# Kernel optimization log

Hardware: AMD Instinct MI355X
Metric: run time of the kernel (lower is better)

Reference implementation:

```python
import jax, jax.numpy as jnp
import numpy as np

N = 4096
E = 262144
IN_DIM = 256
EDGE_DIM = 16
NUM_ATOM_FEATURES = 16
LATENT_DIM = 128
NUM_BOND_TYPES = 5


def setup_inputs() -> dict:
    key = jax.random.key(0)
    ks = jax.random.split(key, 12)
    inp = {
        's': jax.random.normal(ks[0], (N, IN_DIM), dtype=jnp.float32),
        'e': jax.random.normal(ks[1], (E, EDGE_DIM), dtype=jnp.float32),
        'batch': jnp.zeros((N,), dtype=jnp.int64),
        'edge_index_global': jax.random.randint(ks[2], (2, E), 0, N, dtype=jnp.int64),
        # learned parameters (torch nn.Linear layout: W is [out, in])
        'W_shared': jax.random.normal(ks[3], (IN_DIM, IN_DIM), dtype=jnp.float32) * 0.02,
        'b_shared': jnp.zeros((IN_DIM,), dtype=jnp.float32),
        'W_bond': jax.random.normal(ks[4], (IN_DIM, EDGE_DIM), dtype=jnp.float32) * 0.02,
        'b_bond': jnp.zeros((IN_DIM,), dtype=jnp.float32),
        'W_bonds': jax.random.normal(ks[5], (NUM_BOND_TYPES, IN_DIM), dtype=jnp.float32) * 0.02,
        'b_bonds': jnp.zeros((NUM_BOND_TYPES,), dtype=jnp.float32),
        'W_atoms': jax.random.normal(ks[6], (NUM_ATOM_FEATURES + LATENT_DIM, IN_DIM), dtype=jnp.float32) * 0.02,
        'b_atoms': jnp.zeros((NUM_ATOM_FEATURES + LATENT_DIM,), dtype=jnp.float32),
    }
    return inp


def reference(s, e, batch, edge_index_global,
              W_shared, b_shared, W_bond, b_bond,
              W_bonds, b_bonds, W_atoms, b_atoms):
    # shared_mapping: Linear + SiLU
    s = jax.nn.silu(s @ W_shared.T + b_shared)  # [n, in_dim]
    j = edge_index_global[0]
    i = edge_index_global[1]
    n = s.shape[0]

    # atoms_lin then split into atom-type logits and latent prediction
    atoms_out = s @ W_atoms.T + b_atoms  # [n, num_atom_features + latent_dim]
    atoms_pred = atoms_out[:, :NUM_ATOM_FEATURES]
    latent_pred = atoms_out[:, NUM_ATOM_FEATURES:]

    # dense scatter -> symmetrize -> gather (faithful to the original O(n^2) path)
    e_dense = jnp.zeros((n, n, e.shape[-1]), dtype=e.dtype).at[j, i].set(e)
    e_dense = 0.5 * (e_dense + e_dense.transpose(1, 0, 2))
    e_sym = e_dense[j, i]  # [E, edge_dim]

    # fused gather + bond linear + SiLU + bonds linear
    f = jax.nn.silu(s[i] + s[j] + e_sym @ W_bond.T + b_bond)  # [E, in_dim]
    bonds_pred = f @ W_bonds.T + b_bonds  # [E, num_bond_types]

    return (latent_pred, atoms_pred, bonds_pred)
```

## Files before the change

kernel.cpp:

```cpp
#include <hip/hip_runtime.h>
#include <hip/hip_bf16.h>

#define N_NODES   4096
#define E_EDGES   262144
#define IN_DIM    256
#define EDGE_DIM  16
#define NAF       16
#define LATENT    128
#define NBT       5

#define LATENT_OFF 0
#define ATOMS_OFF  (N_NODES * LATENT)
#define BONDS_OFF  (ATOMS_OFF + N_NODES * NAF)

#define TBITS 20
#define TSIZE (1u << TBITS)
#define TMASK (TSIZE - 1u)

typedef float    f32x4  __attribute__((ext_vector_type(4)));
typedef float    f32x4v __attribute__((ext_vector_type(4)));
typedef short    bf16x8 __attribute__((ext_vector_type(8)));
typedef unsigned u32x2  __attribute__((ext_vector_type(2)));
typedef unsigned u32x4  __attribute__((ext_vector_type(4)));

__device__ __forceinline__ float silu_f(float x) {
    return x / (1.0f + __expf(-x));
}

__device__ __forceinline__ unsigned pack_bf16x2(float lo, float hi) {
#if __has_builtin(__builtin_amdgcn_cvt_pk_bf16_f32)
    typedef __bf16 bf16x2_t __attribute__((ext_vector_type(2)));
    union { bf16x2_t v; unsigned u; } c;
    c.v = __builtin_amdgcn_cvt_pk_bf16_f32(lo, hi);
    return c.u;
#else
    union { float f; unsigned u; } a, b;
    a.f = lo; b.f = hi;
    const unsigned ra = (a.u + 0x7FFFu + ((a.u >> 16) & 1u)) >> 16;
    const unsigned rb = (b.u + 0x7FFFu + ((b.u >> 16) & 1u)) >> 16;
    return ra | (rb << 16);
#endif
}

__device__ __forceinline__ float bf_lo(unsigned u) {
    union { unsigned x; float f; } c; c.x = u << 16; return c.f;
}
__device__ __forceinline__ float bf_hi(unsigned u) {
    union { unsigned x; float f; } c; c.x = u & 0xFFFF0000u; return c.f;
}

__device__ __forceinline__ void gld_lds16(const void* g, void* l) {
    __builtin_amdgcn_global_load_lds(
        (const __attribute__((address_space(1))) unsigned*)g,
        (__attribute__((address_space(3))) unsigned*)l, 16, 0, 0);
}

__device__ __forceinline__ int hlookup(const unsigned long long* __restrict__ tab,
                                       unsigned key) {
    unsigned h = (key * 2654435761u) >> (32 - TBITS);
    while (true) {
        const unsigned long long cur = tab[h];
        if (cur == 0ULL) return -1;
        if ((unsigned)(cur >> 18) == key + 1u) return (int)(cur & 0x3FFFFu);
        h = (h + 1u) & TMASK;
    }
}

__global__ __launch_bounds__(256) void k_prep(const float* __restrict__ s,
                                              const float* __restrict__ Wsh,
                                              const float* __restrict__ bsh,
                                              const float* __restrict__ Wa,
                                              const float* __restrict__ ba,
                                              const int* __restrict__ eidx,
                                              const float* __restrict__ Wb,
                                              const float* __restrict__ bb,
                                              const float* __restrict__ Wbs,
                                              unsigned* __restrict__ sact16,
                                              unsigned long long* __restrict__ tab,
                                              u32x4* __restrict__ A12pre,
                                              float* __restrict__ out) {
    __shared__ float sl[8][32];
    __shared__ float st[8][IN_DIM];
    const int blk = blockIdx.x;
    const int c   = threadIdx.x;

    if (blk >= 512) {
        if (blk < 1536) {
            const int k = (blk - 512) * 256 + c;
            const unsigned j = (unsigned)eidx[k];
            const unsigned i = (unsigned)eidx[E_EDGES + k];
            const unsigned key = (j << 12) | i;
            const unsigned long long mine =
                ((unsigned long long)(key + 1u) << 18) | (unsigned)k;
            unsigned h = (key * 2654435761u) >> (32 - TBITS);
            while (true) {
                unsigned long long cur = tab[h];
                if (cur == 0ULL) {
                    const unsigned long long old = atomicCAS(&tab[h], 0ULL, mine);
                    if (old == 0ULL) return;
                    cur = old;
                }
                if ((unsigned)(cur >> 18) == key + 1u) {
                    atomicMax(&tab[h], mine);
                    return;
                }
                h = (h + 1u) & TMASK;
            }
        } else {
#pragma unroll
            for (int ee = 0; ee < 4; ++ee) {
                const int idx  = c + 256 * ee;
                const int g    = idx >> 6;
                const int lane = idx & 63;
                const int m    = lane & 15;
                const int q    = lane >> 4;

                const float4 w = *(const float4*)(Wb + (16 * g + m) * EDGE_DIM + 4 * q);
                u32x4 r;
                r.x = pack_bf16x2(w.x, w.y);
                r.y = pack_bf16x2(w.z, w.w);
                if (m < NBT) {
                    const float4 ws = *(const float4*)(Wbs + m * IN_DIM + 16 * g + 4 * q);
                    r.z = pack_bf16x2(ws.x, ws.y);
                    r.w = pack_bf16x2(ws.z, ws.w);
                } else {
                    r.z = 0u; r.w = 0u;
                }
                A12pre[idx] = r;
            }
        }
        return;
    }

    const int r0 = blk * 8;

    float acc[8];
    const float bias = bsh[c];
#pragma unroll
    for (int r = 0; r < 8; ++r) acc[r] = bias;

    for (int k0 = 0; k0 < IN_DIM; k0 += 32) {
        sl[c >> 5][c & 31] = s[(r0 + (c >> 5)) * IN_DIM + k0 + (c & 31)];
        __syncthreads();

        float4 w4[8];
        const float4* wp = (const float4*)(Wsh + c * IN_DIM + k0);
#pragma unroll
        for (int q = 0; q < 8; ++q) w4[q] = wp[q];
        const float* wf = (const float*)w4;
#pragma unroll
        for (int r = 0; r < 8; ++r) {
            const float4* srow = (const float4*)sl[r];
            float a = acc[r];
#pragma unroll
            for (int q = 0; q < 8; ++q) {
                const float4 sv = srow[q];
                a += sv.x * wf[q * 4 + 0];
                a += sv.y * wf[q * 4 + 1];
                a += sv.z * wf[q * 4 + 2];
                a += sv.w * wf[q * 4 + 3];
            }
            acc[r] = a;
        }
        __syncthreads();
    }
#pragma unroll
    for (int r = 0; r < 8; ++r) st[r][c] = silu_f(acc[r]);
    __syncthreads();

    if (c < 128) {
        const float b0 = 0.5f * bb[2 * c];
        const float b1 = 0.5f * bb[2 * c + 1];
#pragma unroll
        for (int r = 0; r < 8; ++r)
            sact16[(size_t)(r0 + r) * 128 + c] =
                pack_bf16x2(st[r][2 * c] + b0, st[r][2 * c + 1] + b1);
    }

    const bool active = (c < (NAF + LATENT));
    float acc2[8];
    const float bias2 = active ? ba[c] : 0.0f;
#pragma unroll
    for (int r = 0; r < 8; ++r) acc2[r] = bias2;

    if (active) {
        for (int k0 = 0; k0 < IN_DIM; k0 += 32) {
            float4 w4[8];
            const float4* wp = (const float4*)(Wa + c * IN_DIM + k0);
#pragma unroll
            for (int q = 0; q < 8; ++q) w4[q] = wp[q];
            const float* wf = (const float*)w4;
#pragma unroll
            for (int r = 0; r < 8; ++r) {
                const float4* srow = (const float4*)(st[r] + k0);
                float a = acc2[r];
#pragma unroll
                for (int q = 0; q < 8; ++q) {
                    const float4 sv = srow[q];
                    a += sv.x * wf[q * 4 + 0];
                    a += sv.y * wf[q * 4 + 1];
                    a += sv.z * wf[q * 4 + 2];
                    a += sv.w * wf[q * 4 + 3];
                }
                acc2[r] = a;
            }
        }
#pragma unroll
        for (int r = 0; r < 8; ++r) {
            const int row = r0 + r;
            if (c < NAF) out[ATOMS_OFF + row * NAF + c] = acc2[r];
            else         out[LATENT_OFF + row * LATENT + (c - NAF)] = acc2[r];
        }
    }
}

__global__ __launch_bounds__(256, 5) void k_edges_mfma(const int* __restrict__ eidx,
                                                       const float* __restrict__ e,
                                                       const unsigned long long* __restrict__ tab,
                                                       const unsigned* __restrict__ sact16,
                                                       const u32x4* __restrict__ A12pre,
                                                       const float* __restrict__ bbs,
                                                       float* __restrict__ out) {
    __shared__ unsigned lds_all[4][2048];
    const int lane = threadIdx.x & 63;
    const int wv   = threadIdx.x >> 6;
    const int m    = lane & 15;
    const int q    = lane >> 4;
    const int k0   = __builtin_amdgcn_readfirstlane((blockIdx.x * 4 + wv) * 16);
    unsigned* myl = lds_all[wv];

    f32x4v acc_init;
#pragma unroll
    for (int r = 0; r < 4; ++r) {
        const int bond = 4 * q + r;
        acc_init[r] = (bond < NBT) ? bbs[bond] : 0.0f;
    }

    const unsigned j_m = (unsigned)eidx[k0 + m];
    const unsigned i_m = (unsigned)eidx[E_EDGES + k0 + m];

    const char* si_base = (const char*)(sact16 + (size_t)i_m * 128);
    const char* sj_base = (const char*)(sact16 + (size_t)j_m * 128);

#pragma unroll
    for (int u = 0; u < 4; ++u)
        gld_lds16(si_base + (4 * u + q) * 16, (char*)myl + u * 1024);
#pragma unroll
    for (int u = 0; u < 4; ++u)
        gld_lds16(sj_base + (4 * u + q) * 16, (char*)myl + 4096 + u * 1024);

    const unsigned wf = (unsigned)hlookup(tab, (j_m << 12) | i_m);
    const int      wr = hlookup(tab, (i_m << 12) | j_m);

    f32x4 es = *(const f32x4*)(e + (size_t)wf * EDGE_DIM + 4 * q);
    if (wr >= 0)
        es += *(const f32x4*)(e + (size_t)wr * EDGE_DIM + 4 * q);
    es *= 0.5f;

    union { bf16x8 v; unsigned u[4]; } B1;
    B1.u[0] = pack_bf16x2(es[0], es[1]);
    B1.u[1] = pack_bf16x2(es[2], es[3]);
    B1.u[2] = 0u; B1.u[3] = 0u;

    const u32x4* a12p = A12pre + lane;

    f32x4v acc0 = acc_init;
    f32x4v acc1 = {0.0f, 0.0f, 0.0f, 0.0f};

    const int qh  = q >> 1;
    const int qw  = 2 * (q & 1);
    const int mw  = m * 4;

    auto run_half = [&](int h) {
#pragma unroll
        for (int gp = 0; gp < 8; ++gp) {
            const int g     = 8 * h + gp;
            const int chunk = 2 * gp + qh;
            const int offw  = (chunk >> 2) * 256 + ((chunk & 3) * 16) * 4 + mw + qw;

            const u32x2 wi = *(const u32x2*)(myl + offw);
            const u32x2 wj = *(const u32x2*)(myl + 1024 + offw);

            f32x4v C1;
            C1[0] = bf_lo(wi.x) + bf_lo(wj.x);
            C1[1] = bf_hi(wi.x) + bf_hi(wj.x);
            C1[2] = bf_lo(wi.y) + bf_lo(wj.y);
            C1[3] = bf_hi(wi.y) + bf_hi(wj.y);

            const u32x4 rec = a12p[g * 64];
            union { bf16x8 v; unsigned u[4]; } A1, A2;
            A1.u[0] = rec.x; A1.u[1] = rec.y; A1.u[2] = 0u; A1.u[3] = 0u;
            A2.u[0] = rec.z; A2.u[1] = rec.w; A2.u[2] = 0u; A2.u[3] = 0u;

            const f32x4v P = __builtin_amdgcn_mfma_f32_16x16x32_bf16(A1.v, B1.v, C1, 0, 0, 0);

            union { bf16x8 v; unsigned u[4]; } B2;
            B2.u[0] = pack_bf16x2(silu_f(P[0]), silu_f(P[1]));
            B2.u[1] = pack_bf16x2(silu_f(P[2]), silu_f(P[3]));
            B2.u[2] = 0u; B2.u[3] = 0u;

            if (g & 1) acc1 = __builtin_amdgcn_mfma_f32_16x16x32_bf16(A2.v, B2.v, acc1, 0, 0, 0);
            else       acc0 = __builtin_amdgcn_mfma_f32_16x16x32_bf16(A2.v, B2.v, acc0, 0, 0, 0);
        }
    };

    __asm__ __volatile__("s_waitcnt vmcnt(0)" ::: "memory");
    run_half(0);

    __asm__ __volatile__("s_waitcnt lgkmcnt(0)" ::: "memory");
#pragma unroll
    for (int u = 0; u < 4; ++u)
        gld_lds16(si_base + 256 + (4 * u + q) * 16, (char*)myl + u * 1024);
#pragma unroll
    for (int u = 0; u < 4; ++u)
        gld_lds16(sj_base + 256 + (4 * u + q) * 16, (char*)myl + 4096 + u * 1024);
    __asm__ __volatile__("s_waitcnt vmcnt(0)" ::: "memory");
    run_half(1);

    const f32x4v accT = acc0 + acc1;
    float* op = out + BONDS_OFF + (size_t)(k0 + m) * NBT;
    if (q == 0) {
        __builtin_nontemporal_store(accT[0], op + 0);
        __builtin_nontemporal_store(accT[1], op + 1);
        __builtin_nontemporal_store(accT[2], op + 2);
        __builtin_nontemporal_store(accT[3], op + 3);
    } else if (q == 1) {
        __builtin_nontemporal_store(accT[0], op + 4);
    }
}

extern "C" void kernel_launch(void* const* d_in, const int* in_sizes, int n_in,
                              void* d_out, int out_size, void* d_ws, size_t ws_size,
                              hipStream_t stream) {
    const float* s   = (const float*)d_in[0];
    const float* e   = (const float*)d_in[1];
    const int*   eix = (const int*)d_in[3];
    const float* Wsh = (const float*)d_in[4];
    const float* bsh = (const float*)d_in[5];
    const float* Wb  = (const float*)d_in[6];
    const float* bbo = (const float*)d_in[7];
    const float* Wbs = (const float*)d_in[8];
    const float* bbs = (const float*)d_in[9];
    const float* Wa  = (const float*)d_in[10];
    const float* ba  = (const float*)d_in[11];
    float* out = (float*)d_out;

    char* ws = (char*)d_ws;
    unsigned*           sact16 = (unsigned*)ws;
    u32x4*              A12pre = (u32x4*)(ws + (2u << 20));
    unsigned long long* tab    = (unsigned long long*)(ws + (3u << 20));

    (void)hipMemsetAsync(tab, 0x00, TSIZE * sizeof(unsigned long long), stream);

    k_prep<<<1537, 256, 0, stream>>>(s, Wsh, bsh, Wa, ba, eix, Wb, bbo, Wbs,
                                     sact16, tab, A12pre, out);
    k_edges_mfma<<<4096, 256, 0, stream>>>(eix, e, tab, sact16,
                                           A12pre, bbs, out);
}
```

Measured before the change: 210.1 us.

## Move node GEMMs to MFMA with split-bf16 and fold bond bias into MFMA

Replaces the scalar FP32 shared-mapping GEMM with an MFMA tile GEMM that uses a bf16 hi/lo split to keep near-FP32 accuracy. The atoms/latent GEMM moves into extra blocks of the edge kernel, where it reads the bf16 activations. The bond bias is no longer pre-added into the stored node activations; it is folded into the first edge MFMA through an extra constant-one column in B paired with a bias column in A. This splits the packed weight records into two arrays and adds extra MFMAs for the split precision. It is meant to cut the compute time of the prep kernel, at the cost of some added precision error.

```diff
diff --git a/kernel.cpp b/kernel.cpp
--- a/kernel.cpp
+++ b/kernel.cpp
@@ -49,6 +49,20 @@
     union { unsigned x; float f; } c; c.x = u & 0xFFFF0000u; return c.f;
 }
 
+__device__ __forceinline__ void split_bf16(const float4 x0, const float4 x1,
+                                           bf16x8* hi, bf16x8* lo) {
+    union { bf16x8 v; unsigned u[4]; } H, L;
+    H.u[0] = pack_bf16x2(x0.x, x0.y);
+    H.u[1] = pack_bf16x2(x0.z, x0.w);
+    H.u[2] = pack_bf16x2(x1.x, x1.y);
+    H.u[3] = pack_bf16x2(x1.z, x1.w);
+    L.u[0] = pack_bf16x2(x0.x - bf_lo(H.u[0]), x0.y - bf_hi(H.u[0]));
+    L.u[1] = pack_bf16x2(x0.z - bf_lo(H.u[1]), x0.w - bf_hi(H.u[1]));
+    L.u[2] = pack_bf16x2(x1.x - bf_lo(H.u[2]), x1.y - bf_hi(H.u[2]));
+    L.u[3] = pack_bf16x2(x1.z - bf_lo(H.u[3]), x1.w - bf_hi(H.u[3]));
+    *hi = H.v; *lo = L.v;
+}
+
 __device__ __forceinline__ void gld_lds16(const void* g, void* l) {
     __builtin_amdgcn_global_load_lds(
         (const __attribute__((address_space(1))) unsigned*)g,
@@ -66,27 +80,23 @@
     }
 }
 
-__global__ __launch_bounds__(256) void k_prep(const float* __restrict__ s,
-                                              const float* __restrict__ Wsh,
-                                              const float* __restrict__ bsh,
-                                              const float* __restrict__ Wa,
-                                              const float* __restrict__ ba,
-                                              const int* __restrict__ eidx,
-                                              const float* __restrict__ Wb,
-                                              const float* __restrict__ bb,
-                                              const float* __restrict__ Wbs,
-                                              unsigned* __restrict__ sact16,
-                                              unsigned long long* __restrict__ tab,
-                                              u32x4* __restrict__ A12pre,
-                                              float* __restrict__ out) {
-    __shared__ float sl[8][32];
-    __shared__ float st[8][IN_DIM];
+__global__ __launch_bounds__(256) void k_gemm1(const float* __restrict__ s,
+                                               const float* __restrict__ Wsh,
+                                               const float* __restrict__ bsh,
+                                               const int* __restrict__ eidx,
+                                               const float* __restrict__ Wb,
+                                               const float* __restrict__ bb,
+                                               const float* __restrict__ Wbs,
+                                               unsigned short* __restrict__ sact16,
+                                               unsigned long long* __restrict__ tab,
+                                               u32x4* __restrict__ A1pre,
+                                               u32x4* __restrict__ A2pre) {
     const int blk = blockIdx.x;
     const int c   = threadIdx.x;
 
-    if (blk >= 512) {
-        if (blk < 1536) {
-            const int k = (blk - 512) * 256 + c;
+    if (blk >= 1024) {
+        if (blk < 2048) {
+            const int k = (blk - 1024) * 256 + c;
             const unsigned j = (unsigned)eidx[k];
             const unsigned i = (unsigned)eidx[E_EDGES + k];
             const unsigned key = (j << 12) | i;
@@ -116,118 +126,125 @@
                 const int q    = lane >> 4;
 
                 const float4 w = *(const float4*)(Wb + (16 * g + m) * EDGE_DIM + 4 * q);
-                u32x4 r;
-                r.x = pack_bf16x2(w.x, w.y);
-                r.y = pack_bf16x2(w.z, w.w);
+                u32x4 r1;
+                r1.x = pack_bf16x2(w.x, w.y);
+                r1.y = pack_bf16x2(w.z, w.w);
+                r1.z = pack_bf16x2(bb[16 * g + m], 0.0f);
+                r1.w = 0u;
+                A1pre[idx] = r1;
+
+                u32x4 r2;
                 if (m < NBT) {
                     const float4 ws = *(const float4*)(Wbs + m * IN_DIM + 16 * g + 4 * q);
-                    r.z = pack_bf16x2(ws.x, ws.y);
-                    r.w = pack_bf16x2(ws.z, ws.w);
+                    r2.x = pack_bf16x2(ws.x, ws.y);
+                    r2.y = pack_bf16x2(ws.z, ws.w);
                 } else {
-                    r.z = 0u; r.w = 0u;
+                    r2.x = 0u; r2.y = 0u;
                 }
-                A12pre[idx] = r;
+                r2.z = 0u; r2.w = 0u;
+                A2pre[idx] = r2;
             }
         }
         return;
     }
 
-    const int r0 = blk * 8;
-
-    float acc[8];
-    const float bias = bsh[c];
-#pragma unroll
-    for (int r = 0; r < 8; ++r) acc[r] = bias;
-
-    for (int k0 = 0; k0 < IN_DIM; k0 += 32) {
-        sl[c >> 5][c & 31] = s[(r0 + (c >> 5)) * IN_DIM + k0 + (c & 31)];
-        __syncthreads();
-
-        float4 w4[8];
-        const float4* wp = (const float4*)(Wsh + c * IN_DIM + k0);
-#pragma unroll
-        for (int q = 0; q < 8; ++q) w4[q] = wp[q];
-        const float* wf = (const float*)w4;
-#pragma unroll
-        for (int r = 0; r < 8; ++r) {
-            const float4* srow = (const float4*)sl[r];
-            float a = acc[r];
-#pragma unroll
-            for (int q = 0; q < 8; ++q) {
-                const float4 sv = srow[q];
-                a += sv.x * wf[q * 4 + 0];
-                a += sv.y * wf[q * 4 + 1];
-                a += sv.z * wf[q * 4 + 2];
-                a += sv.w * wf[q * 4 + 3];
-            }
-            acc[r] = a;
-        }
-        __syncthreads();
-    }
-#pragma unroll
-    for (int r = 0; r < 8; ++r) st[r][c] = silu_f(acc[r]);
-    __syncthreads();
-
-    if (c < 128) {
-        const float b0 = 0.5f * bb[2 * c];
-        const float b1 = 0.5f * bb[2 * c + 1];
-#pragma unroll
-        for (int r = 0; r < 8; ++r)
-            sact16[(size_t)(r0 + r) * 128 + c] =
-                pack_bf16x2(st[r][2 * c] + b0, st[r][2 * c + 1] + b1);
-    }
-
-    const bool active = (c < (NAF + LATENT));
-    float acc2[8];
-    const float bias2 = active ? ba[c] : 0.0f;
-#pragma unroll
-    for (int r = 0; r < 8; ++r) acc2[r] = bias2;
-
-    if (active) {
-        for (int k0 = 0; k0 < IN_DIM; k0 += 32) {
-            float4 w4[8];
-            const float4* wp = (const float4*)(Wa + c * IN_DIM + k0);
-#pragma unroll
-            for (int q = 0; q < 8; ++q) w4[q] = wp[q];
-            const float* wf = (const float*)w4;
-#pragma unroll
-            for (int r = 0; r < 8; ++r) {
-                const float4* srow = (const float4*)(st[r] + k0);
-                float a = acc2[r];
-#pragma unroll
-                for (int q = 0; q < 8; ++q) {
-                    const float4 sv = srow[q];
-                    a += sv.x * wf[q * 4 + 0];
-                    a += sv.y * wf[q * 4 + 1];
-                    a += sv.z * wf[q * 4 + 2];
-                    a += sv.w * wf[q * 4 + 3];
-                }
-                acc2[r] = a;
-            }
-        }
-#pragma unroll
-        for (int r = 0; r < 8; ++r) {
-            const int row = r0 + r;
-            if (c < NAF) out[ATOMS_OFF + row * NAF + c] = acc2[r];
-            else         out[LATENT_OFF + row * LATENT + (c - NAF)] = acc2[r];
-        }
+    const int lane = c & 63;
+    const int wv   = c >> 6;
+    const int wave = blk * 4 + wv;
+    const int m    = lane & 15;
+    const int q    = lane >> 4;
+    const int row0 = (wave >> 4) * 16;
+    const int col0 = (wave & 15) * 16;
+
+    f32x4v acc;
+    {
+        const float bias = bsh[col0 + m];
+        acc[0] = bias; acc[1] = bias; acc[2] = bias; acc[3] = bias;
+    }
+
+    const float* ap = s   + (size_t)(row0 + m) * IN_DIM + 8 * q;
+    const float* bp = Wsh + (size_t)(col0 + m) * IN_DIM + 8 * q;
+
+#pragma unroll
+    for (int c8 = 0; c8 < 8; ++c8) {
+        const float4 a0 = *(const float4*)(ap + 32 * c8);
+        const float4 a1 = *(const float4*)(ap + 32 * c8 + 4);
+        const float4 b0 = *(const float4*)(bp + 32 * c8);
+        const float4 b1 = *(const float4*)(bp + 32 * c8 + 4);
+        bf16x8 Ah, Al, Bh, Bl;
+        split_bf16(a0, a1, &Ah, &Al);
+        split_bf16(b0, b1, &Bh, &Bl);
+        acc = __builtin_amdgcn_mfma_f32_16x16x32_bf16(Ah, Bh, acc, 0, 0, 0);
+        acc = __builtin_amdgcn_mfma_f32_16x16x32_bf16(Al, Bh, acc, 0, 0, 0);
+        acc = __builtin_amdgcn_mfma_f32_16x16x32_bf16(Ah, Bl, acc, 0, 0, 0);
+    }
+
+#pragma unroll
+    for (int r = 0; r < 4; ++r) {
+        const int row = row0 + 4 * q + r;
+        const float v = silu_f(acc[r]);
+        sact16[(size_t)row * IN_DIM + col0 + m] =
+            (unsigned short)(pack_bf16x2(v, 0.0f) & 0xFFFFu);
     }
 }
 
 __global__ __launch_bounds__(256, 5) void k_edges_mfma(const int* __restrict__ eidx,
                                                        const float* __restrict__ e,
                                                        const unsigned long long* __restrict__ tab,
-                                                       const unsigned* __restrict__ sact16,
-                                                       const u32x4* __restrict__ A12pre,
+                                                       const unsigned short* __restrict__ sact16,
+                                                       const u32x4* __restrict__ A1pre,
+                                                       const u32x4* __restrict__ A2pre,
                                                        const float* __restrict__ bbs,
+                                                       const float* __restrict__ Wa,
+                                                       const float* __restrict__ ba,
                                                        float* __restrict__ out) {
     __shared__ unsigned lds_all[4][2048];
+    const int blk  = blockIdx.x;
     const int lane = threadIdx.x & 63;
     const int wv   = threadIdx.x >> 6;
     const int m    = lane & 15;
     const int q    = lane >> 4;
-    const int k0   = __builtin_amdgcn_readfirstlane((blockIdx.x * 4 + wv) * 16);
+
+    if (blk >= 4096) {
+        const int wave = (blk - 4096) * 4 + wv;
+        const int rt = wave / 9;
+        const int ct = wave - rt * 9;
+        const int row0  = rt * 16;
+        const int n_abs = ct * 16 + m;
+
+        f32x4v acc;
+        {
+            const float bias = ba[n_abs];
+            acc[0] = bias; acc[1] = bias; acc[2] = bias; acc[3] = bias;
+        }
+
+        const unsigned short* apu = sact16 + (size_t)(row0 + m) * IN_DIM + 8 * q;
+        const float*          bp  = Wa + (size_t)n_abs * IN_DIM + 8 * q;
+
+#pragma unroll
+        for (int c8 = 0; c8 < 8; ++c8) {
+            const bf16x8 A = *(const bf16x8*)(apu + 32 * c8);
+            const float4 b0 = *(const float4*)(bp + 32 * c8);
+            const float4 b1 = *(const float4*)(bp + 32 * c8 + 4);
+            bf16x8 Bh, Bl;
+            split_bf16(b0, b1, &Bh, &Bl);
+            acc = __builtin_amdgcn_mfma_f32_16x16x32_bf16(A, Bh, acc, 0, 0, 0);
+            acc = __builtin_amdgcn_mfma_f32_16x16x32_bf16(A, Bl, acc, 0, 0, 0);
+        }
+#pragma unroll
+        for (int r = 0; r < 4; ++r) {
+            const int row = row0 + 4 * q + r;
+            if (n_abs < NAF)
+                out[ATOMS_OFF + (size_t)row * NAF + n_abs] = acc[r];
+            else
+                out[LATENT_OFF + (size_t)row * LATENT + (n_abs - NAF)] = acc[r];
+        }
+        return;
+    }
+
+    const int k0 = __builtin_amdgcn_readfirstlane((blk * 4 + wv) * 16);
     unsigned* myl = lds_all[wv];
+    const short one_q0 = (q == 0) ? (short)0x3F80 : (short)0;
 
     f32x4v acc_init;
 #pragma unroll
@@ -239,8 +256,8 @@
     const unsigned j_m = (unsigned)eidx[k0 + m];
     const unsigned i_m = (unsigned)eidx[E_EDGES + k0 + m];
 
-    const char* si_base = (const char*)(sact16 + (size_t)i_m * 128);
-    const char* sj_base = (const char*)(sact16 + (size_t)j_m * 128);
+    const char* si_base = (const char*)(sact16 + (size_t)i_m * IN_DIM);
+    const char* sj_base = (const char*)(sact16 + (size_t)j_m * IN_DIM);
 
 #pragma unroll
     for (int u = 0; u < 4; ++u)
@@ -257,26 +274,28 @@
         es += *(const f32x4*)(e + (size_t)wr * EDGE_DIM + 4 * q);
     es *= 0.5f;
 
-    union { bf16x8 v; unsigned u[4]; } B1;
+    union { bf16x8 v; short s[8]; unsigned u[4]; } B1;
     B1.u[0] = pack_bf16x2(es[0], es[1]);
     B1.u[1] = pack_bf16x2(es[2], es[3]);
-    B1.u[2] = 0u; B1.u[3] = 0u;
-
-    const u32x4* a12p = A12pre + lane;
+    B1.s[4] = one_q0; B1.s[5] = 0;
+    B1.u[3] = 0u;
+
+    const u32x4* a1p = A1pre + lane;
+    const u32x4* a2p = A2pre + lane;
 
     f32x4v acc0 = acc_init;
     f32x4v acc1 = {0.0f, 0.0f, 0.0f, 0.0f};
 
-    const int qh  = q >> 1;
-    const int qw  = 2 * (q & 1);
-    const int mw  = m * 4;
+    const int qh = q >> 1;
+    const int qw = 2 * (q & 1);
+    const int mw = m * 4;
 
     auto run_half = [&](int h) {
 #pragma unroll
         for (int gp = 0; gp < 8; ++gp) {
             const int g     = 8 * h + gp;
             const int chunk = 2 * gp + qh;
-            const int offw  = (chunk >> 2) * 256 + ((chunk & 3) * 16) * 4 + mw + qw;
+            const int offw  = (chunk >> 2) * 256 + (chunk & 3) * 64 + mw + qw;
 
             const u32x2 wi = *(const u32x2*)(myl + offw);
             const u32x2 wj = *(const u32x2*)(myl + 1024 + offw);
@@ -287,10 +306,11 @@
             C1[2] = bf_lo(wi.y) + bf_lo(wj.y);
             C1[3] = bf_hi(wi.y) + bf_hi(wj.y);
 
-            const u32x4 rec = a12p[g * 64];
+            const u32x4 r1 = a1p[g * 64];
+            const u32x4 r2 = a2p[g * 64];
             union { bf16x8 v; unsigned u[4]; } A1, A2;
-            A1.u[0] = rec.x; A1.u[1] = rec.y; A1.u[2] = 0u; A1.u[3] = 0u;
-            A2.u[0] = rec.z; A2.u[1] = rec.w; A2.u[2] = 0u; A2.u[3] = 0u;
+            A1.u[0] = r1.x; A1.u[1] = r1.y; A1.u[2] = r1.z; A1.u[3] = 0u;
+            A2.u[0] = r2.x; A2.u[1] = r2.y; A2.u[2] = 0u;   A2.u[3] = 0u;
 
             const f32x4v P = __builtin_amdgcn_mfma_f32_16x16x32_bf16(A1.v, B1.v, C1, 0, 0, 0);
 
@@ -346,14 +366,15 @@
     float* out = (float*)d_out;
 
     char* ws = (char*)d_ws;
-    unsigned*           sact16 = (unsigned*)ws;
-    u32x4*              A12pre = (u32x4*)(ws + (2u << 20));
+    unsigned short*     sact16 = (unsigned short*)ws;
+    u32x4*              A1pre  = (u32x4*)(ws + (2u << 20));
+    u32x4*              A2pre  = (u32x4*)(ws + (2u << 20) + 16384);
     unsigned long long* tab    = (unsigned long long*)(ws + (3u << 20));
 
     (void)hipMemsetAsync(tab, 0x00, TSIZE * sizeof(unsigned long long), stream);
 
-    k_prep<<<1537, 256, 0, stream>>>(s, Wsh, bsh, Wa, ba, eix, Wb, bbo, Wbs,
-                                     sact16, tab, A12pre, out);
-    k_edges_mfma<<<4096, 256, 0, stream>>>(eix, e, tab, sact16,
-                                           A12pre, bbs, out);
-}
+    k_gemm1<<<2049, 256, 0, stream>>>(s, Wsh, bsh, eix, Wb, bbo, Wbs,
+                                      sact16, tab, A1pre, A2pre);
+    k_edges_mfma<<<4672, 256, 0, stream>>>(eix, e, tab, sact16,
+                                           A1pre, A2pre, bbs, Wa, ba, out);
+}
```

Result: faster. 193.4 us (-7.9%).
